# Kernel tuning notes

Measured on AMD Instinct MI355X. Metric: run time of the kernel, lower is better.

Reference implementation:

```python
import jax, jax.numpy as jnp
import numpy as np

EPS = 1e-5  # torch InstanceNorm3d default eps


def setup_inputs() -> dict:
    key = jax.random.key(0)
    ks = jax.random.split(key, 7)
    B, C, H, W, D = 2, 128, 48, 48, 48
    c_m, c_n = 128, 64
    return {
        "x": jax.random.normal(ks[0], (B, C, H, W, D), dtype=jnp.float32),
        "WA": jax.random.normal(ks[1], (c_m, C), dtype=jnp.float32) * (1.0 / np.sqrt(C)),
        "bA": jax.random.normal(ks[2], (c_m,), dtype=jnp.float32) * 0.01,
        "WB": jax.random.normal(ks[3], (c_n, C), dtype=jnp.float32) * (1.0 / np.sqrt(C)),
        "bB": jax.random.normal(ks[4], (c_n,), dtype=jnp.float32) * 0.01,
        "WV": jax.random.normal(ks[5], (c_n, C), dtype=jnp.float32) * (1.0 / np.sqrt(C)),
        "bV": jax.random.normal(ks[6], (c_n,), dtype=jnp.float32) * 0.01,
    }


def reference(x, WA, bA, WB, bB, WV, bV):
    B, C, H, W, D = x.shape
    L = H * W * D
    xf = x.reshape(B, C, L)
    # 1x1x1 Conv3d projections == per-voxel linear over channels
    A = jnp.einsum('bcl,mc->bml', xf, WA) + bA[None, :, None]   # (B, c_m, L)
    Bm = jnp.einsum('bcl,nc->bnl', xf, WB) + bB[None, :, None]  # (B, c_n, L)
    V = jnp.einsum('bcl,nc->bnl', xf, WV) + bV[None, :, None]   # (B, c_n, L)
    # attention maps: softmax over spatial positions
    attn_maps = jax.nn.softmax(Bm, axis=-1)                     # (B, c_n, L)
    # global descriptors: A @ attn_maps^T
    G = jnp.einsum('bml,bnl->bmn', A, attn_maps)                # (B, c_m, c_n)
    # attention vectors: softmax over c_n (channel) dim
    attn_vec = jax.nn.softmax(V, axis=1)                        # (B, c_n, L)
    Z = jnp.einsum('bmn,bnl->bml', G, attn_vec)                 # (B, c_m, L)
    # InstanceNorm3d (affine=False, biased variance) per (batch, channel)
    mean = jnp.mean(Z, axis=-1, keepdims=True)
    var = jnp.var(Z, axis=-1, keepdims=True)
    Zn = (Z - mean) * jax.lax.rsqrt(var + EPS)
    return Zn.reshape(B, Z.shape[1], H, W, D)
```

## Files before the change

kernel.cpp:

```cpp
#include <hip/hip_runtime.h>

#define LTOT 110592
#define EPSV 1e-5f

typedef _Float16 f16;
typedef __attribute__((ext_vector_type(4))) _Float16 f16x4;
typedef __attribute__((ext_vector_type(8))) _Float16 f16x8;
typedef __attribute__((ext_vector_type(4))) float f32x4;

#define MFMA16(a, b, c) __builtin_amdgcn_mfma_f32_16x16x32_f16(a, b, c, 0, 0, 0)

__device__ __forceinline__ f16x8 ld_w8(const float* p) {
  const float4 a = *(const float4*)p;
  const float4 b = *(const float4*)(p + 4);
  f16x8 f;
  f[0] = (f16)a.x; f[1] = (f16)a.y; f[2] = (f16)a.z; f[3] = (f16)a.w;
  f[4] = (f16)b.x; f[5] = (f16)b.y; f[6] = (f16)b.z; f[7] = (f16)b.w;
  return f;
}

__global__ __launch_bounds__(256, 2) void p1_proj_m(
    const float* __restrict__ x,
    const float* __restrict__ WB_, const float* __restrict__ bB_,
    const float* __restrict__ WV_, const float* __restrict__ bV_,
    f16* __restrict__ av_g, float* __restrict__ mpart, float* __restrict__ separt)
{
  __shared__ __align__(16) f16 XT[64 * 128];
  __shared__ __align__(16) f16 XC[128 * 64];
  __shared__ __align__(16) f16 EL[64 * 64];
  __shared__ __align__(16) f16 AVT[64 * 64];
  __shared__ float colp[4][64];
  const int tid = threadIdx.x, b = blockIdx.y, blk = blockIdx.x;
  const int ln = tid & 63, w = tid >> 6, g = ln >> 4;

  const int nB = w * 16 + (ln & 15);
  f16x8 wbf[4], wvf[4];
  #pragma unroll
  for (int ks = 0; ks < 4; ++ks) {
    wbf[ks] = ld_w8(&WB_[nB * 128 + ks * 32 + g * 8]);
    wvf[ks] = ld_w8(&WV_[nB * 128 + ks * 32 + g * 8]);
  }
  const float sB = bB_[nB];
  float biasV[4];
  #pragma unroll
  for (int r = 0; r < 4; ++r) biasV[r] = bV_[w * 16 + g * 4 + r];

  f32x4 macc[8];
  #pragma unroll
  for (int i = 0; i < 8; ++i) macc[i] = (f32x4){0.f, 0.f, 0.f, 0.f};
  float se = 0.f;

  const int xt_co = tid & 15, xt_lq = tid >> 4;
  const int xc_lo = tid & 7,  xc_c4 = tid >> 3;
  const size_t xb = (size_t)b * 128 * LTOT;

  for (int t = 0; t < 4; ++t) {
    const int l0 = (blk * 4 + t) * 64;
    __syncthreads();
    {
      float4 xr[8];
      #pragma unroll
      for (int j = 0; j < 8; ++j)
        xr[j] = *(const float4*)&x[xb + (size_t)(xt_co * 8 + j) * LTOT + l0 + xt_lq * 4];
      #pragma unroll
      for (int i = 0; i < 4; ++i) {
        const int l = xt_lq * 4 + i;
        f16x8 v;
        #pragma unroll
        for (int j = 0; j < 8; ++j) v[j] = (f16)(((const float*)&xr[j])[i]);
        *(f16x8*)&XT[l * 128 + ((xt_co * 8) ^ ((l & 7) << 3))] = v;
      }
    }
    #pragma unroll
    for (int i = 0; i < 4; ++i) {
      const int c = xc_c4 * 4 + i;
      const float4 a = *(const float4*)&x[xb + (size_t)c * LTOT + l0 + xc_lo * 8];
      const float4 d = *(const float4*)&x[xb + (size_t)c * LTOT + l0 + xc_lo * 8 + 4];
      f16x8 v;
      v[0] = (f16)a.x; v[1] = (f16)a.y; v[2] = (f16)a.z; v[3] = (f16)a.w;
      v[4] = (f16)d.x; v[5] = (f16)d.y; v[6] = (f16)d.z; v[7] = (f16)d.w;
      *(f16x8*)&XC[c * 64 + ((xc_lo * 8) ^ ((c & 7) << 3))] = v;
    }
    __syncthreads();
    f32x4 aB[4], aV[4];
    #pragma unroll
    for (int lt = 0; lt < 4; ++lt) {
      aB[lt] = (f32x4){0.f, 0.f, 0.f, 0.f};
      aV[lt] = (f32x4){0.f, 0.f, 0.f, 0.f};
      const int l = lt * 16 + (ln & 15);
      #pragma unroll
      for (int ks = 0; ks < 4; ++ks) {
        const f16x8 xf = *(const f16x8*)&XT[l * 128 + (((ks * 4 + g) * 8) ^ ((l & 7) << 3))];
        aB[lt] = MFMA16(xf, wbf[ks], aB[lt]);
        aV[lt] = MFMA16(wvf[ks], xf, aV[lt]);
      }
    }
    #pragma unroll
    for (int lt = 0; lt < 4; ++lt) {
      f16x4 ev4;
      #pragma unroll
      for (int r = 0; r < 4; ++r) {
        const float e = __expf(aB[lt][r] + sB);
        se += e;
        ev4[r] = (f16)e;
      }
      const int lq = lt * 16 + g * 4;
      *(f16x4*)&EL[nB * 64 + (lq ^ ((nB & 7) << 3))] = ev4;
    }
    float cs[4];
    #pragma unroll
    for (int ct = 0; ct < 4; ++ct) {
      f16x4 av4;
      float s = 0.f;
      #pragma unroll
      for (int r = 0; r < 4; ++r) {
        const float e = __expf(aV[ct][r] + biasV[r]);
        s += e;
        av4[r] = (f16)e;
      }
      cs[ct] = s;
      const int l = ct * 16 + (ln & 15);
      *(f16x4*)&AVT[l * 64 + ((w * 16 + g * 4) ^ ((l & 7) << 3))] = av4;
    }
    #pragma unroll
    for (int ct = 0; ct < 4; ++ct) {
      cs[ct] += __shfl_xor(cs[ct], 16);
      cs[ct] += __shfl_xor(cs[ct], 32);
    }
    {
      const float v = (g == 0) ? cs[0] : (g == 1) ? cs[1] : (g == 2) ? cs[2] : cs[3];
      colp[w][g * 16 + (ln & 15)] = v;
    }
    __syncthreads();
    {
      const int l = tid >> 2, q = tid & 3;
      const float rs = 1.f / (colp[0][l] + colp[1][l] + colp[2][l] + colp[3][l]);
      f16x8 a0 = *(const f16x8*)&AVT[l * 64 + ((q * 16) ^ ((l & 7) << 3))];
      f16x8 a1 = *(const f16x8*)&AVT[l * 64 + ((q * 16 + 8) ^ ((l & 7) << 3))];
      #pragma unroll
      for (int j = 0; j < 8; ++j) {
        a0[j] = (f16)((float)a0[j] * rs);
        a1[j] = (f16)((float)a1[j] * rs);
      }
      f16* gp = av_g + ((size_t)b * LTOT + l0 + l) * 64 + q * 16;
      *(f16x8*)&gp[0] = a0;
      *(f16x8*)&gp[8] = a1;
    }
    {
      f16x8 el[2];
      #pragma unroll
      for (int ks = 0; ks < 2; ++ks)
        el[ks] = *(const f16x8*)&EL[nB * 64 + ((ks * 32 + g * 8) ^ ((nB & 7) << 3))];
      #pragma unroll
      for (int cblk = 0; cblk < 8; ++cblk) {
        const int c = cblk * 16 + (ln & 15);
        #pragma unroll
        for (int ks = 0; ks < 2; ++ks) {
          const f16x8 xcf = *(const f16x8*)&XC[c * 64 + ((ks * 32 + g * 8) ^ ((c & 7) << 3))];
          macc[cblk] = MFMA16(el[ks], xcf, macc[cblk]);
        }
      }
    }
  }
  float* mp = mpart + (size_t)(b * 432 + blk) * 8192;
  #pragma unroll
  for (int cblk = 0; cblk < 8; ++cblk)
    #pragma unroll
    for (int r = 0; r < 4; ++r)
      mp[(w * 16 + g * 4 + r) * 128 + cblk * 16 + (ln & 15)] = macc[cblk][r];
  se += __shfl_xor(se, 16);
  se += __shfl_xor(se, 32);
  if (ln < 16) separt[(size_t)(b * 432 + blk) * 64 + w * 16 + ln] = se;
}

__global__ void p2a(const float* __restrict__ mpart, const float* __restrict__ separt,
                    float* __restrict__ mpart2, float* __restrict__ sesum)
{
  const int b = blockIdx.y, bx = blockIdx.x, tid = threadIdx.x;
  if (bx < 256) {
    const int seg = bx >> 5, chunk = bx & 31;
    const int idx = chunk * 256 + tid;
    float s = 0.f;
    for (int j = 0; j < 54; ++j)
      s += mpart[(size_t)(b * 432 + seg * 54 + j) * 8192 + idx];
    mpart2[(size_t)(b * 8 + seg) * 8192 + idx] = s;
  } else if (tid < 64) {
    float s = 0.f;
    for (int k = 0; k < 432; ++k) s += separt[(size_t)(b * 432 + k) * 64 + tid];
    sesum[b * 64 + tid] = s;
  }
}

__global__ void p2a2(const float* __restrict__ mpart2, float* __restrict__ msum)
{
  const int b = blockIdx.y;
  const int idx = blockIdx.x * 256 + threadIdx.x;
  float s = 0.f;
  #pragma unroll
  for (int k = 0; k < 8; ++k) s += mpart2[(size_t)(b * 8 + k) * 8192 + idx];
  msum[(size_t)b * 8192 + idx] = s;
}

__global__ void p2b(const float* __restrict__ WA_, const float* __restrict__ bA_,
                    const float* __restrict__ msum, const float* __restrict__ sesum,
                    float* __restrict__ g32, f16* __restrict__ g16)
{
  const int b = blockIdx.y;
  const int idx = blockIdx.x * 256 + threadIdx.x;
  const int m = idx >> 6, n = idx & 63;
  float s = 0.f;
  #pragma unroll 4
  for (int c = 0; c < 128; ++c) s += WA_[m * 128 + c] * msum[(size_t)b * 8192 + n * 128 + c];
  const float gv = s / sesum[b * 64 + n] + bA_[m];
  g32[(size_t)b * 8192 + m * 64 + n] = gv;
  g16[(size_t)b * 8192 + m * 64 + (n ^ ((m & 7) << 3))] = (f16)gv;
}

__global__ __launch_bounds__(256, 2) void p3_cov(
    const f16* __restrict__ av_g, float* __restrict__ cpart, float* __restrict__ mupart)
{
  __shared__ __align__(16) f16 AV[64 * 64];
  const int tid = threadIdx.x, b = blockIdx.y, blk = blockIdx.x;
  const int ln = tid & 63, w = tid >> 6, g = ln >> 4;
  const int nq4 = (tid & 15) * 4, lq4 = (tid >> 4) * 4;
  const int nmu = tid >> 2, qmu = tid & 3;

  f32x4 cacc[4];
  #pragma unroll
  for (int j = 0; j < 4; ++j) cacc[j] = (f32x4){0.f, 0.f, 0.f, 0.f};
  float muacc = 0.f;

  for (int t = 0; t < 8; ++t) {
    const int l0 = (blk * 8 + t) * 64;
    __syncthreads();
    {
      f16x4 rd[4];
      #pragma unroll
      for (int i = 0; i < 4; ++i)
        rd[i] = *(const f16x4*)&av_g[((size_t)b * LTOT + l0 + lq4 + i) * 64 + nq4];
      #pragma unroll
      for (int j = 0; j < 4; ++j) {
        const int n = nq4 + j;
        f16x4 wr;
        #pragma unroll
        for (int i = 0; i < 4; ++i) wr[i] = rd[i][j];
        *(f16x4*)&AV[n * 64 + (lq4 ^ ((n & 7) << 3))] = wr;
      }
    }
    __syncthreads();
    {
      const f16x8 a0 = *(const f16x8*)&AV[nmu * 64 + ((qmu * 16) ^ ((nmu & 7) << 3))];
      const f16x8 a1 = *(const f16x8*)&AV[nmu * 64 + ((qmu * 16 + 8) ^ ((nmu & 7) << 3))];
      #pragma unroll
      for (int j = 0; j < 8; ++j) muacc += (float)a0[j] + (float)a1[j];
    }
    const int nA = w * 16 + (ln & 15);
    f16x8 caf[2];
    #pragma unroll
    for (int ks = 0; ks < 2; ++ks)
      caf[ks] = *(const f16x8*)&AV[nA * 64 + ((ks * 32 + g * 8) ^ ((nA & 7) << 3))];
    #pragma unroll
    for (int nct = 0; nct < 4; ++nct) {
      const int nb = nct * 16 + (ln & 15);
      #pragma unroll
      for (int ks = 0; ks < 2; ++ks) {
        const f16x8 cbf = *(const f16x8*)&AV[nb * 64 + ((ks * 32 + g * 8) ^ ((nb & 7) << 3))];
        cacc[nct] = MFMA16(caf[ks], cbf, cacc[nct]);
      }
    }
  }
  float* cp = cpart + (size_t)(b * 216 + blk) * 4096;
  #pragma unroll
  for (int nct = 0; nct < 4; ++nct)
    #pragma unroll
    for (int r = 0; r < 4; ++r)
      cp[(w * 16 + g * 4 + r) * 64 + nct * 16 + (ln & 15)] = cacc[nct][r];
  muacc += __shfl_xor(muacc, 1);
  muacc += __shfl_xor(muacc, 2);
  if (qmu == 0) mupart[(size_t)(b * 216 + blk) * 64 + nmu] = muacc;
}

__global__ void p4a(const float* __restrict__ cpart, const float* __restrict__ mupart,
                    float* __restrict__ csum, float* __restrict__ musum)
{
  const int b = blockIdx.y, bx = blockIdx.x, tid = threadIdx.x;
  if (bx < 64) {
    const int idx = bx * 64 + (tid >> 2), q = tid & 3;
    float s = 0.f;
    for (int k = q; k < 216; k += 4) s += cpart[(size_t)(b * 216 + k) * 4096 + idx];
    s += __shfl_xor(s, 1);
    s += __shfl_xor(s, 2);
    if (q == 0) csum[(size_t)b * 4096 + idx] = s;
  } else if (tid < 64) {
    float s = 0.f;
    for (int k = 0; k < 216; ++k) s += mupart[(size_t)(b * 216 + k) * 64 + tid];
    musum[b * 64 + tid] = s;
  }
}

__global__ void p4b(const float* __restrict__ csum, const float* __restrict__ musum,
                    const float* __restrict__ g32, float* __restrict__ mr)
{
  __shared__ __align__(16) float CL[4096];
  __shared__ __align__(16) float GLs[32 * 68];
  __shared__ float MUL[64];
  const int tid = threadIdx.x, b = blockIdx.y, bx = blockIdx.x;
  #pragma unroll
  for (int k = 0; k < 16; ++k) CL[k * 256 + tid] = csum[(size_t)b * 4096 + k * 256 + tid];
  #pragma unroll
  for (int k = 0; k < 8; ++k) {
    const int idx = k * 256 + tid;
    const int m_ = idx >> 6, n_ = idx & 63;
    GLs[m_ * 68 + n_] = g32[(size_t)b * 8192 + (bx * 32 + m_) * 64 + n_];
  }
  if (tid < 64) MUL[tid] = musum[b * 64 + tid];
  __syncthreads();
  const int mrow = (tid >> 3) * 68, oct = tid & 7;
  float q = 0.f;
  #pragma unroll
  for (int q4 = 0; q4 < 2; ++q4) {
    const int npb = oct * 8 + q4 * 4;
    float t0 = 0.f, t1 = 0.f, t2 = 0.f, t3 = 0.f;
    #pragma unroll 8
    for (int n = 0; n < 64; ++n) {
      const float4 cv = *(const float4*)&CL[n * 64 + npb];
      const float gv = GLs[mrow + n];
      t0 += gv * cv.x; t1 += gv * cv.y; t2 += gv * cv.z; t3 += gv * cv.w;
    }
    const float4 gq = *(const float4*)&GLs[mrow + npb];
    q += t0 * gq.x + t1 * gq.y + t2 * gq.z + t3 * gq.w;
  }
  q += __shfl_xor(q, 1); q += __shfl_xor(q, 2); q += __shfl_xor(q, 4);
  if (oct == 0) {
    float meanq = 0.f;
    #pragma unroll 8
    for (int n = 0; n < 64; ++n) meanq += GLs[mrow + n] * MUL[n];
    const int m = bx * 32 + (tid >> 3);
    const float mean = meanq / (float)LTOT;
    const float var = fmaxf(q / (float)LTOT - mean * mean, 0.f);
    mr[(b * 128 + m) * 2] = mean;
    mr[(b * 128 + m) * 2 + 1] = rsqrtf(var + EPSV);
  }
}

__global__ __launch_bounds__(256, 2) void p5_z(
    const f16* __restrict__ av_g, const f16* __restrict__ g16,
    const float* __restrict__ mr, float* __restrict__ out)
{
  __shared__ __align__(16) f16 AVT[64 * 64];
  const int tid = threadIdx.x, b = blockIdx.y, blk = blockIdx.x;
  const int ln = tid & 63, w = tid >> 6, g = ln >> 4;
  const int lst = tid & 63, pst = tid >> 6;

  f16x8 gf[2][2];
  float mean_[2][4], rsig_[2][4];
  #pragma unroll
  for (int mct = 0; mct < 2; ++mct) {
    const int mA = w * 32 + mct * 16 + (ln & 15);
    #pragma unroll
    for (int ks = 0; ks < 2; ++ks)
      gf[mct][ks] = *(const f16x8*)&g16[(size_t)b * 8192 + mA * 64 +
                                        (((ks * 4 + g) * 8) ^ ((mA & 7) << 3))];
    #pragma unroll
    for (int r = 0; r < 4; ++r) {
      const int m = w * 32 + mct * 16 + g * 4 + r;
      mean_[mct][r] = mr[(b * 128 + m) * 2];
      rsig_[mct][r] = mr[(b * 128 + m) * 2 + 1];
    }
  }

  for (int t = 0; t < 4; ++t) {
    const int l0 = (blk * 4 + t) * 64;
    __syncthreads();
    {
      const f16* gp = av_g + ((size_t)b * LTOT + l0 + lst) * 64 + pst * 16;
      const f16x8 a0 = *(const f16x8*)&gp[0];
      const f16x8 a1 = *(const f16x8*)&gp[8];
      *(f16x8*)&AVT[lst * 64 + ((pst * 16) ^ ((lst & 7) << 3))] = a0;
      *(f16x8*)&AVT[lst * 64 + ((pst * 16 + 8) ^ ((lst & 7) << 3))] = a1;
    }
    __syncthreads();
    #pragma unroll
    for (int lt = 0; lt < 4; ++lt) {
      const int l = lt * 16 + (ln & 15);
      f16x8 avf[2];
      #pragma unroll
      for (int ks = 0; ks < 2; ++ks)
        avf[ks] = *(const f16x8*)&AVT[l * 64 + (((ks * 4 + g) * 8) ^ ((l & 7) << 3))];
      #pragma unroll
      for (int mct = 0; mct < 2; ++mct) {
        f32x4 z = {0.f, 0.f, 0.f, 0.f};
        #pragma unroll
        for (int ks = 0; ks < 2; ++ks) z = MFMA16(gf[mct][ks], avf[ks], z);
        #pragma unroll
        for (int r = 0; r < 4; ++r) {
          const int m = w * 32 + mct * 16 + g * 4 + r;
          out[(size_t)(b * 128 + m) * LTOT + l0 + l] =
              (z[r] - mean_[mct][r]) * rsig_[mct][r];
        }
      }
    }
  }
}

extern "C" void kernel_launch(void* const* d_in, const int* in_sizes, int n_in,
                              void* d_out, int out_size, void* d_ws, size_t ws_size,
                              hipStream_t stream)
{
  const float* x  = (const float*)d_in[0];
  const float* WA = (const float*)d_in[1];
  const float* bA = (const float*)d_in[2];
  const float* WB = (const float*)d_in[3];
  const float* bB = (const float*)d_in[4];
  const float* WV = (const float*)d_in[5];
  const float* bV = (const float*)d_in[6];
  float* out = (float*)d_out;

  float* w = (float*)d_ws;
  float* mpart  = w;
  float* mpart2 = mpart + 7077888;
  float* separt = mpart2 + 131072;
  float* msum   = separt + 55296;
  float* sesum  = msum + 16384;
  float* g32    = sesum + 128;
  f16*   g16f   = (f16*)(g32 + 16384);
  f16*   av_g   = g16f + 16384;
  float* cpart  = (float*)(av_g + 14155776);
  float* mupart = cpart + 1769472;
  float* csum   = mupart + 27648;
  float* musum  = csum + 8192;
  float* mr     = musum + 128;

  p1_proj_m<<<dim3(432, 2), 256, 0, stream>>>(x, WB, bB, WV, bV, av_g, mpart, separt);
  p2a<<<dim3(257, 2), 256, 0, stream>>>(mpart, separt, mpart2, sesum);
  p2a2<<<dim3(32, 2), 256, 0, stream>>>(mpart2, msum);
  p2b<<<dim3(32, 2), 256, 0, stream>>>(WA, bA, msum, sesum, g32, g16f);
  p3_cov<<<dim3(216, 2), 256, 0, stream>>>(av_g, cpart, mupart);
  p4a<<<dim3(65, 2), 256, 0, stream>>>(cpart, mupart, csum, musum);
  p4b<<<dim3(4, 2), 256, 0, stream>>>(csum, musum, g32, mr);
  p5_z<<<dim3(432, 2), 256, 0, stream>>>(av_g, g16f, mr, out);
}
```

Before: 137.8 us.

## Load x once per tile, build both LDS layouts from registers, prefetch next tile

The x tile is now read from global memory once per 64-position step instead of twice. Both the transposed XT layout and the channel-major XC layout are built from the same registers, with a new XOR swizzle for XC. The load for the next tile is issued after the barrier, so it can overlap the MFMA work of the current tile. XT also gets padding, which raises LDS use and adds register pressure from holding the prefetched values.

```diff
diff --git a/kernel.cpp b/kernel.cpp
--- a/kernel.cpp
+++ b/kernel.cpp
@@ -9,6 +9,7 @@
 typedef __attribute__((ext_vector_type(4))) float f32x4;
 
 #define MFMA16(a, b, c) __builtin_amdgcn_mfma_f32_16x16x32_f16(a, b, c, 0, 0, 0)
+#define SWC(c) ((((c) ^ ((c) >> 3)) & 7) << 3)
 
 __device__ __forceinline__ f16x8 ld_w8(const float* p) {
   const float4 a = *(const float4*)p;
@@ -25,7 +26,7 @@
     const float* __restrict__ WV_, const float* __restrict__ bV_,
     f16* __restrict__ av_g, float* __restrict__ mpart, float* __restrict__ separt)
 {
-  __shared__ __align__(16) f16 XT[64 * 128];
+  __shared__ __align__(16) f16 XT[64 * 128 + 2240];
   __shared__ __align__(16) f16 XC[128 * 64];
   __shared__ __align__(16) f16 EL[64 * 64];
   __shared__ __align__(16) f16 AVT[64 * 64];
@@ -50,38 +51,43 @@
   for (int i = 0; i < 8; ++i) macc[i] = (f32x4){0.f, 0.f, 0.f, 0.f};
   float se = 0.f;
 
-  const int xt_co = tid & 15, xt_lq = tid >> 4;
-  const int xc_lo = tid & 7,  xc_c4 = tid >> 3;
+  const int co = tid & 15, LQ = tid >> 4;
   const size_t xb = (size_t)b * 128 * LTOT;
+
+  float4 xr[8];
+  {
+    const int l0 = blk * 256;
+    #pragma unroll
+    for (int j = 0; j < 8; ++j)
+      xr[j] = *(const float4*)&x[xb + (size_t)(co * 8 + j) * LTOT + l0 + LQ * 4];
+  }
 
   for (int t = 0; t < 4; ++t) {
     const int l0 = (blk * 4 + t) * 64;
     __syncthreads();
-    {
-      float4 xr[8];
+    #pragma unroll
+    for (int i = 0; i < 4; ++i) {
+      const int l = LQ * 4 + i;
+      f16x8 v;
+      #pragma unroll
+      for (int j = 0; j < 8; ++j) v[j] = (f16)(((const float*)&xr[j])[i]);
+      *(f16x8*)&XT[l * 128 + ((co * 8) ^ ((l & 7) << 3))] = v;
+    }
+    #pragma unroll
+    for (int j = 0; j < 8; ++j) {
+      const int c = co * 8 + j;
+      f16x4 q;
+      q[0] = (f16)xr[j].x; q[1] = (f16)xr[j].y;
+      q[2] = (f16)xr[j].z; q[3] = (f16)xr[j].w;
+      *(f16x4*)&XC[c * 64 + ((LQ * 4) ^ SWC(c))] = q;
+    }
+    __syncthreads();
+    if (t < 3) {
+      const int l0n = l0 + 64;
       #pragma unroll
       for (int j = 0; j < 8; ++j)
-        xr[j] = *(const float4*)&x[xb + (size_t)(xt_co * 8 + j) * LTOT + l0 + xt_lq * 4];
-      #pragma unroll
-      for (int i = 0; i < 4; ++i) {
-        const int l = xt_lq * 4 + i;
-        f16x8 v;
-        #pragma unroll
-        for (int j = 0; j < 8; ++j) v[j] = (f16)(((const float*)&xr[j])[i]);
-        *(f16x8*)&XT[l * 128 + ((xt_co * 8) ^ ((l & 7) << 3))] = v;
-      }
-    }
-    #pragma unroll
-    for (int i = 0; i < 4; ++i) {
-      const int c = xc_c4 * 4 + i;
-      const float4 a = *(const float4*)&x[xb + (size_t)c * LTOT + l0 + xc_lo * 8];
-      const float4 d = *(const float4*)&x[xb + (size_t)c * LTOT + l0 + xc_lo * 8 + 4];
-      f16x8 v;
-      v[0] = (f16)a.x; v[1] = (f16)a.y; v[2] = (f16)a.z; v[3] = (f16)a.w;
-      v[4] = (f16)d.x; v[5] = (f16)d.y; v[6] = (f16)d.z; v[7] = (f16)d.w;
-      *(f16x8*)&XC[c * 64 + ((xc_lo * 8) ^ ((c & 7) << 3))] = v;
-    }
-    __syncthreads();
+        xr[j] = *(const float4*)&x[xb + (size_t)(co * 8 + j) * LTOT + l0n + LQ * 4];
+    }
     f32x4 aB[4], aV[4];
     #pragma unroll
     for (int lt = 0; lt < 4; ++lt) {
@@ -156,7 +162,7 @@
         const int c = cblk * 16 + (ln & 15);
         #pragma unroll
         for (int ks = 0; ks < 2; ++ks) {
-          const f16x8 xcf = *(const f16x8*)&XC[c * 64 + ((ks * 32 + g * 8) ^ ((c & 7) << 3))];
+          const f16x8 xcf = *(const f16x8*)&XC[c * 64 + ((ks * 32 + g * 8) ^ SWC(c))];
           macc[cblk] = MFMA16(el[ks], xcf, macc[cblk]);
         }
       }
```

Result: faster. 128.4 us (-6.8%).
